# Optimization experiments

Measured on AMD Instinct MI355X. Metric: run time of the kernel, lower is better.

Reference implementation:

```python
import jax, jax.numpy as jnp
import numpy as np

NH, K = 16, 4  # num_heads, num_points


def _ln(x, g, b):
    m = x.mean(-1, keepdims=True)
    v = jnp.var(x, axis=-1, keepdims=True)
    return (x - m) / jnp.sqrt(v + 1e-5) * g + b


def setup_inputs() -> dict:
    key = jax.random.key(0)
    ks = jax.random.split(key, 12)
    B, S, D = 16, 1024, 1024
    HD = D // NH
    def lin(k, fi, fo, scale=1.0):
        return jax.random.normal(k, (fi, fo), jnp.float32) * (scale / np.sqrt(fi))
    z = lambda n: jnp.zeros((n,), jnp.float32)
    return {
        "source": jax.random.normal(ks[0], (B, S, D), jnp.float32),
        "target": jax.random.normal(ks[1], (B, S, D), jnp.float32),
        "Wq": lin(ks[2], D, D), "bq": z(D),
        "Wo1": lin(ks[3], HD, 64), "bo1": z(64),
        "Wo2": lin(ks[4], 64, 2 * K, 0.1), "bo2": z(2 * K),
        "Wa": lin(ks[5], HD, K), "ba": z(K),
        "Wv": lin(ks[6], D, D), "bv": z(D),
        "Wout": lin(ks[7], D, D), "bout": z(D),
        "gq": jnp.ones((D,), jnp.float32), "bq_ln": z(D),
        "gkv": jnp.ones((D,), jnp.float32), "bkv_ln": z(D),
        "gffn": jnp.ones((D,), jnp.float32), "bffn_ln": z(D),
        "W1": lin(ks[8], D, 4 * D), "b1": z(4 * D),
        "W2": lin(ks[9], 4 * D, D), "b2": z(D),
    }


def _forward(source, target, Wq, bq, Wo1, bo1, Wo2, bo2, Wa, ba, Wv, bv,
             Wout, bout, gq, bq_ln, gkv, bkv_ln, gffn, bffn_ln, W1, b1, W2, b2):
    B, S, D = source.shape
    HD = D // NH
    Hs = int(round(S ** 0.5)); Ws = Hs  # S = H*W square grid

    q_norm = _ln(source, gq, bq_ln)
    v_norm = _ln(target, gkv, bkv_ln)
    q = (q_norm @ Wq + bq).reshape(B, S, NH, HD)
    # value map per head: (B, NH, H, W, HD)
    v = (v_norm @ Wv + bv).reshape(B, Hs, Ws, NH, HD).transpose(0, 3, 1, 2, 4)
    v_flat = v.reshape(B, NH, Hs * Ws, HD)

    # learned offsets: tanh(MLP(q)) * 0.5, in normalized [-1,1] coords
    h = jax.nn.relu(q @ Wo1 + bo1)
    off = jnp.tanh((h @ Wo2 + bo2).reshape(B, S, NH, K, 2)) * 0.5

    # reference grid: ref_grid[i*W+j] = (ref_x[j], ref_y[i])
    rx = jnp.linspace(-1.0, 1.0, Ws)
    ry = jnp.linspace(-1.0, 1.0, Hs)
    gx, gy = jnp.meshgrid(rx, ry)  # 'xy' indexing
    ref = jnp.stack([gx, gy], -1).reshape(S, 2)
    pts = ref[None, :, None, None, :] + off  # (B, S, NH, K, 2), last dim = (x, y)

    # grid_sample, bilinear, align_corners=True, padding_mode='zeros'
    x = (pts[..., 0] + 1.0) * 0.5 * (Ws - 1)
    y = (pts[..., 1] + 1.0) * 0.5 * (Hs - 1)
    x = jnp.moveaxis(x, 1, 2)  # (B, NH, S, K)
    y = jnp.moveaxis(y, 1, 2)
    x0 = jnp.floor(x); y0 = jnp.floor(y)
    wx1 = x - x0; wy1 = y - y0
    x0i = x0.astype(jnp.int32); y0i = y0.astype(jnp.int32)

    def gather(xi, yi, w):
        m = (xi >= 0) & (xi <= Ws - 1) & (yi >= 0) & (yi <= Hs - 1)
        idx = jnp.clip(yi, 0, Hs - 1) * Ws + jnp.clip(xi, 0, Ws - 1)
        g = jnp.take_along_axis(v_flat, idx.reshape(B, NH, S * K, 1), axis=2)
        return g.reshape(B, NH, S, K, HD) * (w * m)[..., None]

    sampled = (gather(x0i, y0i, (1.0 - wx1) * (1.0 - wy1))
               + gather(x0i + 1, y0i, wx1 * (1.0 - wy1))
               + gather(x0i, y0i + 1, (1.0 - wx1) * wy1)
               + gather(x0i + 1, y0i + 1, wx1 * wy1))  # (B, NH, S, K, HD)

    attn = jax.nn.softmax(q @ Wa + ba, axis=-1)  # (B, S, NH, K)
    head_out = jnp.einsum('bsnk,bnskd->bsnd', attn, sampled).reshape(B, S, D)

    src = source + (head_out @ Wout + bout)
    f = jax.nn.gelu(_ln(src, gffn, bffn_ln) @ W1 + b1, approximate=False)
    return src + (f @ W2 + b2)


def reference(source, target, Wq, bq, Wo1, bo1, Wo2, bo2, Wa, ba, Wv, bv,
              Wout, bout, gq, bq_ln, gkv, bkv_ln, gffn, bffn_ln, W1, b1, W2, b2):
    return _forward(source, target, Wq, bq, Wo1, bo1, Wo2, bo2, Wa, ba, Wv, bv,
                    Wout, bout, gq, bq_ln, gkv, bkv_ln, gffn, bffn_ln, W1, b1, W2, b2)
```

## Files before the change

kernel.cpp:

```cpp
#include <hip/hip_runtime.h>

typedef __attribute__((ext_vector_type(8))) short short8;
typedef __attribute__((ext_vector_type(4))) float f32x4;

#define DEV __device__ __forceinline__

DEV float bf2f(unsigned short u) { return __uint_as_float(((unsigned)u) << 16); }
DEV unsigned short f2bf(float f) {
  unsigned u = __float_as_uint(f);
  u += 0x7FFF + ((u >> 16) & 1);
  return (unsigned short)(u >> 16);
}

#define GLOAD_LDS16(gptr, lptr)                                                              \
  __builtin_amdgcn_global_load_lds((const __attribute__((address_space(1))) void*)(gptr),   \
                                   (__attribute__((address_space(3))) void*)(lptr), 16, 0, 0)

__global__ __launch_bounds__(256) void wt_transpose_bf16(const float* __restrict__ W,
                                                         unsigned short* __restrict__ Wt,
                                                         int K, int N) {
  __shared__ float t[32][33];
  int k0 = blockIdx.x * 32, n0 = blockIdx.y * 32;
  int tx = threadIdx.x, ty = threadIdx.y;
#pragma unroll
  for (int i = 0; i < 4; ++i)
    t[ty + 8 * i][tx] = W[(long)(k0 + ty + 8 * i) * N + n0 + tx];
  __syncthreads();
#pragma unroll
  for (int i = 0; i < 4; ++i)
    Wt[(long)(n0 + ty + 8 * i) * K + k0 + tx] = f2bf(t[tx][ty + 8 * i]);
}

__global__ __launch_bounds__(256) void ln_to_bf16(const float* __restrict__ x,
                                                  const float* __restrict__ g,
                                                  const float* __restrict__ b,
                                                  unsigned short* __restrict__ y) {
  const long row = blockIdx.x;
  const int tid = threadIdx.x;
  float4 v = *(const float4*)(x + row * 1024 + tid * 4);
  float s = v.x + v.y + v.z + v.w;
  float s2 = v.x * v.x + v.y * v.y + v.z * v.z + v.w * v.w;
#pragma unroll
  for (int o = 32; o > 0; o >>= 1) { s += __shfl_down(s, o); s2 += __shfl_down(s2, o); }
  __shared__ float red[8];
  __shared__ float mv[2];
  int wv = tid >> 6, ln = tid & 63;
  if (ln == 0) { red[wv] = s; red[4 + wv] = s2; }
  __syncthreads();
  if (tid == 0) {
    float a = red[0] + red[1] + red[2] + red[3];
    float q = red[4] + red[5] + red[6] + red[7];
    float mean = a * (1.f / 1024.f);
    mv[0] = mean;
    mv[1] = rsqrtf(q * (1.f / 1024.f) - mean * mean + 1e-5f);
  }
  __syncthreads();
  float mean = mv[0], rstd = mv[1];
  float4 gg = *(const float4*)(g + tid * 4);
  float4 bb = *(const float4*)(b + tid * 4);
  ushort4 o;
  o.x = f2bf((v.x - mean) * rstd * gg.x + bb.x);
  o.y = f2bf((v.y - mean) * rstd * gg.y + bb.y);
  o.z = f2bf((v.z - mean) * rstd * gg.z + bb.z);
  o.w = f2bf((v.w - mean) * rstd * gg.w + bb.w);
  *(ushort4*)(y + row * 1024 + tid * 4) = o;
}

template <int EPI>
__global__ __launch_bounds__(512, 4) void gemm_bf16(const unsigned short* __restrict__ A,
                                                    const unsigned short* __restrict__ Bt,
                                                    const float* __restrict__ bias,
                                                    const float* __restrict__ res,
                                                    void* __restrict__ out,
                                                    int N, int K, int ldb) {
  __shared__ __align__(16) char smem[65536];
  const int tid = threadIdx.x;
  const int wave = tid >> 6, lane = tid & 63;
  const int wm = wave >> 2, wn = wave & 3;
  const long col0 = (long)blockIdx.x * 128;
  const long row0 = (long)blockIdx.y * 128;

  f32x4 acc[4][2];
#pragma unroll
  for (int i = 0; i < 4; ++i)
#pragma unroll
    for (int n = 0; n < 2; ++n) acc[i][n] = f32x4{0.f, 0.f, 0.f, 0.f};

  const int rin = lane >> 4, ch = lane & 15;

  for (int kt = 0; kt < K; kt += 128) {
#pragma unroll
    for (int i = 0; i < 4; ++i) {
      const int c = wave * 4 + i;
      const int r = c * 4 + rin;
      const int kg = ch ^ (r & 15);
      GLOAD_LDS16(A + (row0 + r) * (long)K + kt + kg * 8, smem + c * 1024);
      GLOAD_LDS16(Bt + (col0 + r) * (long)ldb + kt + kg * 8, smem + 32768 + c * 1024);
    }
    asm volatile("s_waitcnt vmcnt(0)" ::: "memory");
    __syncthreads();
#pragma unroll
    for (int ks = 0; ks < 4; ++ks) {
      short8 af[4], bfr[2];
#pragma unroll
      for (int i = 0; i < 4; ++i) {
        const int rowa = wm * 64 + i * 16 + (lane & 15);
        const int pc = (ks * 4 + (lane >> 4)) ^ (rowa & 15);
        af[i] = *(const short8*)(smem + rowa * 256 + pc * 16);
      }
#pragma unroll
      for (int n = 0; n < 2; ++n) {
        const int rowb = wn * 32 + n * 16 + (lane & 15);
        const int pc = (ks * 4 + (lane >> 4)) ^ (rowb & 15);
        bfr[n] = *(const short8*)(smem + 32768 + rowb * 256 + pc * 16);
      }
#pragma unroll
      for (int i = 0; i < 4; ++i)
#pragma unroll
        for (int n = 0; n < 2; ++n)
          acc[i][n] = __builtin_amdgcn_mfma_f32_16x16x32_bf16(af[i], bfr[n], acc[i][n], 0, 0, 0);
    }
    __syncthreads();
  }

  const int lr = lane >> 4, lc = lane & 15;
#pragma unroll
  for (int i = 0; i < 4; ++i) {
#pragma unroll
    for (int n = 0; n < 2; ++n) {
      const long gcol = col0 + wn * 32 + n * 16 + lc;
      const float bvv = (EPI == 5) ? 0.f : bias[gcol];
#pragma unroll
      for (int r = 0; r < 4; ++r) {
        const long grow = row0 + wm * 64 + i * 16 + lr * 4 + r;
        float val = acc[i][n][r] + bvv;
        if (EPI == 0) {
          ((float*)out)[grow * N + gcol] = val;
        } else if (EPI == 1) {
          const int b_ = (int)(grow >> 10), hw = (int)(grow & 1023);
          const int nh = (int)(gcol >> 6), hd = (int)(gcol & 63);
          ((unsigned short*)out)[((long)(b_ * 16 + nh) << 16) + hw * 64 + hd] = f2bf(val);
        } else if (EPI == 2) {
          ((float*)out)[grow * N + gcol] = val + res[grow * N + gcol];
        } else if (EPI == 3) {
          float gl = 0.5f * val * (1.f + erff(val * 0.70710678118654752f));
          ((unsigned short*)out)[grow * N + gcol] = f2bf(gl);
        } else {
          ((float*)out)[grow * N + gcol] = val + res[grow * N + gcol];
        }
      }
    }
  }
}

__global__ __launch_bounds__(256) void offset_attn_mlp(
    const float* __restrict__ qf,
    const float* __restrict__ Wo1, const float* __restrict__ bo1,
    const float* __restrict__ Wo2, const float* __restrict__ bo2,
    const float* __restrict__ Wa, const float* __restrict__ ba,
    float* __restrict__ coords) {
  const int r = blockIdx.x * 256 + threadIdx.x;
  const int s = (r >> 4) & 1023;

  float qr[64];
  const float* qp = qf + (long)r * 64;
#pragma unroll
  for (int i = 0; i < 16; ++i) *(float4*)(qr + 4 * i) = *(const float4*)(qp + 4 * i);

  float off[8];
#pragma unroll
  for (int o = 0; o < 8; ++o) off[o] = bo2[o];

#pragma unroll 1
  for (int jj = 0; jj < 8; ++jj) {
    float hacc[8];
#pragma unroll
    for (int o = 0; o < 8; ++o) hacc[o] = bo1[jj * 8 + o];
#pragma unroll
    for (int i = 0; i < 64; ++i) {
      const float qv = qr[i];
#pragma unroll
      for (int o = 0; o < 8; ++o) hacc[o] = fmaf(qv, Wo1[i * 64 + jj * 8 + o], hacc[o]);
    }
#pragma unroll
    for (int jo = 0; jo < 8; ++jo) {
      const float hj = fmaxf(hacc[jo], 0.f);
      const int j = jj * 8 + jo;
#pragma unroll
      for (int o = 0; o < 8; ++o) off[o] = fmaf(hj, Wo2[j * 8 + o], off[o]);
    }
  }

  float lg[4];
#pragma unroll
  for (int k = 0; k < 4; ++k) lg[k] = ba[k];
#pragma unroll
  for (int i = 0; i < 64; ++i) {
    const float qv = qr[i];
#pragma unroll
    for (int k = 0; k < 4; ++k) lg[k] = fmaf(qv, Wa[i * 4 + k], lg[k]);
  }
  const float mx = fmaxf(fmaxf(lg[0], lg[1]), fmaxf(lg[2], lg[3]));
  const float e0 = expf(lg[0] - mx), e1 = expf(lg[1] - mx), e2 = expf(lg[2] - mx),
              e3 = expf(lg[3] - mx);
  const float inv = 1.f / (e0 + e1 + e2 + e3);

  const float sx = (float)(s & 31), sy = (float)(s >> 5);
  float4 xv, yv, av;
  xv.x = sx + tanhf(off[0]) * 7.75f; yv.x = sy + tanhf(off[1]) * 7.75f;
  xv.y = sx + tanhf(off[2]) * 7.75f; yv.y = sy + tanhf(off[3]) * 7.75f;
  xv.z = sx + tanhf(off[4]) * 7.75f; yv.z = sy + tanhf(off[5]) * 7.75f;
  xv.w = sx + tanhf(off[6]) * 7.75f; yv.w = sy + tanhf(off[7]) * 7.75f;
  av.x = e0 * inv; av.y = e1 * inv; av.z = e2 * inv; av.w = e3 * inv;
  float* cp = coords + (long)r * 16;
  *(float4*)(cp + 0) = xv;
  *(float4*)(cp + 4) = yv;
  *(float4*)(cp + 8) = av;
}

__global__ __launch_bounds__(256) void deform_gather(
    const unsigned short* __restrict__ v_flat, const float* __restrict__ coords,
    unsigned short* __restrict__ head_out) {
  const int tid = threadIdx.x, wave = tid >> 6, lane = tid & 63;
  const int m = blockIdx.x * 4 + wave;
  const int b = m >> 14, nh = (m >> 10) & 15, s = m & 1023;
  const long r = (long)(b * 1024 + s) * 16 + nh;

  float cf = 0.f;
  if (lane < 12) cf = coords[r * 16 + lane];
  const unsigned short* vb = v_flat + ((long)(b * 16 + nh) << 16);

  float o = 0.f;
#pragma unroll
  for (int k = 0; k < 4; ++k) {
    const float xp = __shfl(cf, k), yp = __shfl(cf, 4 + k), ak = __shfl(cf, 8 + k);
    const float x0f = floorf(xp), y0f = floorf(yp);
    const int x0 = (int)x0f, y0 = (int)y0f;
    const float wx1 = xp - x0f, wy1 = yp - y0f;
    const float wx0 = 1.f - wx1, wy0 = 1.f - wy1;
    float smp = 0.f;
#pragma unroll
    for (int cn = 0; cn < 4; ++cn) {
      const int xi = x0 + (cn & 1), yi = y0 + (cn >> 1);
      const float w = (cn & 1 ? wx1 : wx0) * (cn >> 1 ? wy1 : wy0);
      const bool msk = (xi >= 0) & (xi <= 31) & (yi >= 0) & (yi <= 31);
      const int xc = min(max(xi, 0), 31), yc = min(max(yi, 0), 31);
      const float vv = bf2f(vb[(yc * 32 + xc) * 64 + lane]);
      smp = fmaf(vv, msk ? w : 0.f, smp);
    }
    o = fmaf(ak, smp, o);
  }
  head_out[r * 64 + lane] = f2bf(o);
}

extern "C" void kernel_launch(void* const* d_in, const int* in_sizes, int n_in,
                              void* d_out, int out_size, void* d_ws, size_t ws_size,
                              hipStream_t stream) {
  const float* source = (const float*)d_in[0];
  const float* target = (const float*)d_in[1];
  const float* Wq = (const float*)d_in[2];
  const float* bq = (const float*)d_in[3];
  const float* Wo1 = (const float*)d_in[4];
  const float* bo1 = (const float*)d_in[5];
  const float* Wo2 = (const float*)d_in[6];
  const float* bo2 = (const float*)d_in[7];
  const float* Wa = (const float*)d_in[8];
  const float* ba = (const float*)d_in[9];
  const float* Wv = (const float*)d_in[10];
  const float* bv = (const float*)d_in[11];
  const float* Wout = (const float*)d_in[12];
  const float* bout = (const float*)d_in[13];
  const float* gq = (const float*)d_in[14];
  const float* bq_ln = (const float*)d_in[15];
  const float* gkv = (const float*)d_in[16];
  const float* bkv_ln = (const float*)d_in[17];
  const float* gffn = (const float*)d_in[18];
  const float* bffn_ln = (const float*)d_in[19];
  const float* W1 = (const float*)d_in[20];
  const float* b1 = (const float*)d_in[21];
  const float* W2 = (const float*)d_in[22];
  const float* b2 = (const float*)d_in[23];

  char* ws = (char*)d_ws;
  const size_t MB = 1u << 20;
  if (ws_size < 150 * MB) return;

  unsigned short* q_norm = (unsigned short*)(ws + 0);
  unsigned short* v_flat = (unsigned short*)(ws + 0);
  unsigned short* v_norm = (unsigned short*)(ws + 32 * MB);
  float* coords = (float*)(ws + 32 * MB);
  unsigned short* ffn_in = (unsigned short*)(ws + 32 * MB);
  float* qf = (float*)(ws + 64 * MB);
  unsigned short* head_out = (unsigned short*)(ws + 64 * MB);
  unsigned short* f_buf = (unsigned short*)(ws + 64 * MB);
  unsigned short* Wq_t = (unsigned short*)(ws + 128 * MB);
  unsigned short* Wv_t = (unsigned short*)(ws + 130 * MB);
  unsigned short* Wout_t = (unsigned short*)(ws + 132 * MB);
  unsigned short* W1_t = (unsigned short*)(ws + 134 * MB);
  unsigned short* W2_t = (unsigned short*)(ws + 142 * MB);
  float* src = (float*)d_out;

  dim3 tb(32, 8);
  wt_transpose_bf16<<<dim3(32, 32), tb, 0, stream>>>(Wq, Wq_t, 1024, 1024);
  wt_transpose_bf16<<<dim3(32, 32), tb, 0, stream>>>(Wv, Wv_t, 1024, 1024);
  wt_transpose_bf16<<<dim3(32, 32), tb, 0, stream>>>(Wout, Wout_t, 1024, 1024);
  wt_transpose_bf16<<<dim3(32, 128), tb, 0, stream>>>(W1, W1_t, 1024, 4096);
  wt_transpose_bf16<<<dim3(128, 32), tb, 0, stream>>>(W2, W2_t, 4096, 1024);

  ln_to_bf16<<<16384, 256, 0, stream>>>(source, gq, bq_ln, q_norm);
  ln_to_bf16<<<16384, 256, 0, stream>>>(target, gkv, bkv_ln, v_norm);

  gemm_bf16<0><<<dim3(8, 128), 512, 0, stream>>>(q_norm, Wq_t, bq, nullptr, qf, 1024, 1024, 1024);
  gemm_bf16<1><<<dim3(8, 128), 512, 0, stream>>>(v_norm, Wv_t, bv, nullptr, v_flat, 1024, 1024, 1024);

  offset_attn_mlp<<<1024, 256, 0, stream>>>(qf, Wo1, bo1, Wo2, bo2, Wa, ba, coords);
  deform_gather<<<65536, 256, 0, stream>>>(v_flat, coords, head_out);

  gemm_bf16<2><<<dim3(8, 128), 512, 0, stream>>>(head_out, Wout_t, bout, source, src, 1024, 1024, 1024);

  ln_to_bf16<<<16384, 256, 0, stream>>>(src, gffn, bffn_ln, ffn_in);

  gemm_bf16<3><<<dim3(16, 128), 512, 0, stream>>>(ffn_in, W1_t, b1, nullptr, f_buf, 2048, 1024, 1024);
  gemm_bf16<2><<<dim3(8, 128), 512, 0, stream>>>(f_buf, W2_t, b2, src, src, 1024, 2048, 4096);
  gemm_bf16<3><<<dim3(16, 128), 512, 0, stream>>>(ffn_in, W1_t + (long)2048 * 1024, b1 + 2048,
                                                  nullptr, f_buf, 2048, 1024, 1024);
  gemm_bf16<5><<<dim3(8, 128), 512, 0, stream>>>(f_buf, W2_t + 2048, nullptr, src, src, 1024, 2048, 4096);
}
```

Baseline: 786.3 us.

## Switch GEMM to 32x32x16 MFMA with 256x128 tiles and BK=64

```diff
diff --git a/kernel.cpp b/kernel.cpp
--- a/kernel.cpp
+++ b/kernel.cpp
@@ -1,7 +1,7 @@
 #include <hip/hip_runtime.h>
 
 typedef __attribute__((ext_vector_type(8))) short short8;
-typedef __attribute__((ext_vector_type(4))) float f32x4;
+typedef __attribute__((ext_vector_type(16))) float f32x16;
 
 #define DEV __device__ __forceinline__
 
@@ -73,67 +73,74 @@
                                                     const float* __restrict__ res,
                                                     void* __restrict__ out,
                                                     int N, int K, int ldb) {
-  __shared__ __align__(16) char smem[65536];
+  __shared__ __align__(16) char smem[49152];
   const int tid = threadIdx.x;
   const int wave = tid >> 6, lane = tid & 63;
-  const int wm = wave >> 2, wn = wave & 3;
+  const int wm = wave >> 1, wn = wave & 1;
   const long col0 = (long)blockIdx.x * 128;
-  const long row0 = (long)blockIdx.y * 128;
-
-  f32x4 acc[4][2];
-#pragma unroll
-  for (int i = 0; i < 4; ++i)
-#pragma unroll
-    for (int n = 0; n < 2; ++n) acc[i][n] = f32x4{0.f, 0.f, 0.f, 0.f};
-
-  const int rin = lane >> 4, ch = lane & 15;
-
-  for (int kt = 0; kt < K; kt += 128) {
+  const long row0 = (long)blockIdx.y * 256;
+
+  f32x16 acc[2][2];
+#pragma unroll
+  for (int i = 0; i < 2; ++i)
+#pragma unroll
+    for (int n = 0; n < 2; ++n)
+#pragma unroll
+      for (int r = 0; r < 16; ++r) acc[i][n][r] = 0.f;
+
+  const int rin = lane >> 3, ch = lane & 7;
+  const int kg = ch ^ rin;
+
+  for (int kt = 0; kt < K; kt += 64) {
 #pragma unroll
     for (int i = 0; i < 4; ++i) {
       const int c = wave * 4 + i;
-      const int r = c * 4 + rin;
-      const int kg = ch ^ (r & 15);
+      const int r = c * 8 + rin;
       GLOAD_LDS16(A + (row0 + r) * (long)K + kt + kg * 8, smem + c * 1024);
+    }
+#pragma unroll
+    for (int i = 0; i < 2; ++i) {
+      const int c = wave * 2 + i;
+      const int r = c * 8 + rin;
       GLOAD_LDS16(Bt + (col0 + r) * (long)ldb + kt + kg * 8, smem + 32768 + c * 1024);
     }
     asm volatile("s_waitcnt vmcnt(0)" ::: "memory");
     __syncthreads();
 #pragma unroll
     for (int ks = 0; ks < 4; ++ks) {
-      short8 af[4], bfr[2];
-#pragma unroll
-      for (int i = 0; i < 4; ++i) {
-        const int rowa = wm * 64 + i * 16 + (lane & 15);
-        const int pc = (ks * 4 + (lane >> 4)) ^ (rowa & 15);
-        af[i] = *(const short8*)(smem + rowa * 256 + pc * 16);
+      short8 af[2], bfr[2];
+      const int kc = ks * 2 + (lane >> 5);
+#pragma unroll
+      for (int mi = 0; mi < 2; ++mi) {
+        const int rowa = wm * 64 + mi * 32 + (lane & 31);
+        af[mi] = *(const short8*)(smem + rowa * 128 + (kc ^ (rowa & 7)) * 16);
       }
 #pragma unroll
-      for (int n = 0; n < 2; ++n) {
-        const int rowb = wn * 32 + n * 16 + (lane & 15);
-        const int pc = (ks * 4 + (lane >> 4)) ^ (rowb & 15);
-        bfr[n] = *(const short8*)(smem + 32768 + rowb * 256 + pc * 16);
+      for (int ni = 0; ni < 2; ++ni) {
+        const int rowb = wn * 64 + ni * 32 + (lane & 31);
+        bfr[ni] = *(const short8*)(smem + 32768 + rowb * 128 + (kc ^ (rowb & 7)) * 16);
       }
 #pragma unroll
-      for (int i = 0; i < 4; ++i)
-#pragma unroll
-        for (int n = 0; n < 2; ++n)
-          acc[i][n] = __builtin_amdgcn_mfma_f32_16x16x32_bf16(af[i], bfr[n], acc[i][n], 0, 0, 0);
+      for (int mi = 0; mi < 2; ++mi)
+#pragma unroll
+        for (int ni = 0; ni < 2; ++ni)
+          acc[mi][ni] =
+              __builtin_amdgcn_mfma_f32_32x32x16_bf16(af[mi], bfr[ni], acc[mi][ni], 0, 0, 0);
     }
     __syncthreads();
   }
 
-  const int lr = lane >> 4, lc = lane & 15;
-#pragma unroll
-  for (int i = 0; i < 4; ++i) {
-#pragma unroll
-    for (int n = 0; n < 2; ++n) {
-      const long gcol = col0 + wn * 32 + n * 16 + lc;
+  const int lc = lane & 31, lh = lane >> 5;
+#pragma unroll
+  for (int mi = 0; mi < 2; ++mi) {
+#pragma unroll
+    for (int ni = 0; ni < 2; ++ni) {
+      const long gcol = col0 + wn * 64 + ni * 32 + lc;
       const float bvv = (EPI == 5) ? 0.f : bias[gcol];
 #pragma unroll
-      for (int r = 0; r < 4; ++r) {
-        const long grow = row0 + wm * 64 + i * 16 + lr * 4 + r;
-        float val = acc[i][n][r] + bvv;
+      for (int reg = 0; reg < 16; ++reg) {
+        const long grow = row0 + wm * 64 + mi * 32 + (reg & 3) + 8 * (reg >> 2) + 4 * lh;
+        float val = acc[mi][ni][reg] + bvv;
         if (EPI == 0) {
           ((float*)out)[grow * N + gcol] = val;
         } else if (EPI == 1) {
@@ -310,19 +317,19 @@
   ln_to_bf16<<<16384, 256, 0, stream>>>(source, gq, bq_ln, q_norm);
   ln_to_bf16<<<16384, 256, 0, stream>>>(target, gkv, bkv_ln, v_norm);
 
-  gemm_bf16<0><<<dim3(8, 128), 512, 0, stream>>>(q_norm, Wq_t, bq, nullptr, qf, 1024, 1024, 1024);
-  gemm_bf16<1><<<dim3(8, 128), 512, 0, stream>>>(v_norm, Wv_t, bv, nullptr, v_flat, 1024, 1024, 1024);
+  gemm_bf16<0><<<dim3(8, 64), 512, 0, stream>>>(q_norm, Wq_t, bq, nullptr, qf, 1024, 1024, 1024);
+  gemm_bf16<1><<<dim3(8, 64), 512, 0, stream>>>(v_norm, Wv_t, bv, nullptr, v_flat, 1024, 1024, 1024);
 
   offset_attn_mlp<<<1024, 256, 0, stream>>>(qf, Wo1, bo1, Wo2, bo2, Wa, ba, coords);
   deform_gather<<<65536, 256, 0, stream>>>(v_flat, coords, head_out);
 
-  gemm_bf16<2><<<dim3(8, 128), 512, 0, stream>>>(head_out, Wout_t, bout, source, src, 1024, 1024, 1024);
+  gemm_bf16<2><<<dim3(8, 64), 512, 0, stream>>>(head_out, Wout_t, bout, source, src, 1024, 1024, 1024);
 
   ln_to_bf16<<<16384, 256, 0, stream>>>(src, gffn, bffn_ln, ffn_in);
 
-  gemm_bf16<3><<<dim3(16, 128), 512, 0, stream>>>(ffn_in, W1_t, b1, nullptr, f_buf, 2048, 1024, 1024);
-  gemm_bf16<2><<<dim3(8, 128), 512, 0, stream>>>(f_buf, W2_t, b2, src, src, 1024, 2048, 4096);
-  gemm_bf16<3><<<dim3(16, 128), 512, 0, stream>>>(ffn_in, W1_t + (long)2048 * 1024, b1 + 2048,
-                                                  nullptr, f_buf, 2048, 1024, 1024);
-  gemm_bf16<5><<<dim3(8, 128), 512, 0, stream>>>(f_buf, W2_t + 2048, nullptr, src, src, 1024, 2048, 4096);
-}
+  gemm_bf16<3><<<dim3(16, 64), 512, 0, stream>>>(ffn_in, W1_t, b1, nullptr, f_buf, 2048, 1024, 1024);
+  gemm_bf16<2><<<dim3(8, 64), 512, 0, stream>>>(f_buf, W2_t, b2, src, src, 1024, 2048, 4096);
+  gemm_bf16<3><<<dim3(16, 64), 512, 0, stream>>>(ffn_in, W1_t + (long)2048 * 1024, b1 + 2048,
+                                                 nullptr, f_buf, 2048, 1024, 1024);
+  gemm_bf16<5><<<dim3(8, 64), 512, 0, stream>>>(f_buf, W2_t + 2048, nullptr, src, src, 1024, 2048, 4096);
+}
```

New measurement: 766.6 us. -2.5%, faster.

## Add 256x128 GEMM using 32x32x16 MFMA and unsplit FFN when workspace allows

Applied to the files above, without the earlier changes.

```diff
diff --git a/kernel.cpp b/kernel.cpp
--- a/kernel.cpp
+++ b/kernel.cpp
@@ -2,6 +2,7 @@
 
 typedef __attribute__((ext_vector_type(8))) short short8;
 typedef __attribute__((ext_vector_type(4))) float f32x4;
+typedef __attribute__((ext_vector_type(16))) float f32x16;
 
 #define DEV __device__ __forceinline__
 
@@ -64,6 +65,24 @@
   o.z = f2bf((v.z - mean) * rstd * gg.z + bb.z);
   o.w = f2bf((v.w - mean) * rstd * gg.w + bb.w);
   *(ushort4*)(y + row * 1024 + tid * 4) = o;
+}
+
+template <int EPI>
+DEV void epi_store(void* out, const float* res, long grow, long gcol, int N, float val) {
+  if (EPI == 0) {
+    ((float*)out)[grow * N + gcol] = val;
+  } else if (EPI == 1) {
+    const int b_ = (int)(grow >> 10), hw = (int)(grow & 1023);
+    const int nh = (int)(gcol >> 6), hd = (int)(gcol & 63);
+    ((unsigned short*)out)[((long)(b_ * 16 + nh) << 16) + hw * 64 + hd] = f2bf(val);
+  } else if (EPI == 2) {
+    ((float*)out)[grow * N + gcol] = val + res[grow * N + gcol];
+  } else if (EPI == 3) {
+    float gl = 0.5f * val * (1.f + erff(val * 0.70710678118654752f));
+    ((unsigned short*)out)[grow * N + gcol] = f2bf(gl);
+  } else {
+    ((float*)out)[grow * N + gcol] = val + res[grow * N + gcol];
+  }
 }
 
 template <int EPI>
@@ -125,7 +144,7 @@
 
   const int lr = lane >> 4, lc = lane & 15;
 #pragma unroll
-  for (int i = 0; i < 4; ++i) {
+  for (int i = 0; i < 4; ++i)
 #pragma unroll
     for (int n = 0; n < 2; ++n) {
       const long gcol = col0 + wn * 32 + n * 16 + lc;
@@ -133,24 +152,89 @@
 #pragma unroll
       for (int r = 0; r < 4; ++r) {
         const long grow = row0 + wm * 64 + i * 16 + lr * 4 + r;
-        float val = acc[i][n][r] + bvv;
-        if (EPI == 0) {
-          ((float*)out)[grow * N + gcol] = val;
-        } else if (EPI == 1) {
-          const int b_ = (int)(grow >> 10), hw = (int)(grow & 1023);
-          const int nh = (int)(gcol >> 6), hd = (int)(gcol & 63);
-          ((unsigned short*)out)[((long)(b_ * 16 + nh) << 16) + hw * 64 + hd] = f2bf(val);
-        } else if (EPI == 2) {
-          ((float*)out)[grow * N + gcol] = val + res[grow * N + gcol];
-        } else if (EPI == 3) {
-          float gl = 0.5f * val * (1.f + erff(val * 0.70710678118654752f));
-          ((unsigned short*)out)[grow * N + gcol] = f2bf(gl);
-        } else {
-          ((float*)out)[grow * N + gcol] = val + res[grow * N + gcol];
-        }
-      }
-    }
-  }
+        epi_store<EPI>(out, res, grow, gcol, N, acc[i][n][r] + bvv);
+      }
+    }
+}
+
+template <int EPI>
+__global__ __launch_bounds__(512, 4) void gemm32(const unsigned short* __restrict__ A,
+                                                 const unsigned short* __restrict__ Bt,
+                                                 const float* __restrict__ bias,
+                                                 const float* __restrict__ res,
+                                                 void* __restrict__ out,
+                                                 int N, int K, int ldb) {
+  __shared__ __align__(16) char smem[49152];
+  const int tid = threadIdx.x;
+  const int wave = tid >> 6, lane = tid & 63;
+  const int wm = wave >> 1, wn = wave & 1;
+  const long col0 = (long)blockIdx.x * 128;
+  const long row0 = (long)blockIdx.y * 256;
+
+  f32x16 acc[2][2];
+#pragma unroll
+  for (int i = 0; i < 2; ++i)
+#pragma unroll
+    for (int n = 0; n < 2; ++n)
+#pragma unroll
+      for (int r = 0; r < 16; ++r) acc[i][n][r] = 0.f;
+
+  const int rin = lane >> 3, ch = lane & 7;
+
+  for (int kt = 0; kt < K; kt += 64) {
+#pragma unroll
+    for (int i = 0; i < 4; ++i) {
+      const int c = wave * 4 + i;
+      const int r = c * 8 + rin;
+      const int kg = ch ^ ((r >> 1) & 7);
+      GLOAD_LDS16(A + (row0 + r) * (long)K + kt + kg * 8, smem + c * 1024);
+    }
+#pragma unroll
+    for (int i = 0; i < 2; ++i) {
+      const int c = wave * 2 + i;
+      const int r = c * 8 + rin;
+      const int kg = ch ^ ((r >> 1) & 7);
+      GLOAD_LDS16(Bt + (col0 + r) * (long)ldb + kt + kg * 8, smem + 32768 + c * 1024);
+    }
+    asm volatile("s_waitcnt vmcnt(0)" ::: "memory");
+    __syncthreads();
+#pragma unroll
+    for (int ks = 0; ks < 4; ++ks) {
+      short8 af[2], bfr[2];
+      const int kc = ks * 2 + (lane >> 5);
+#pragma unroll
+      for (int mi = 0; mi < 2; ++mi) {
+        const int rowa = wm * 64 + mi * 32 + (lane & 31);
+        af[mi] = *(const short8*)(smem + rowa * 128 + (kc ^ ((rowa >> 1) & 7)) * 16);
+      }
+#pragma unroll
+      for (int ni = 0; ni < 2; ++ni) {
+        const int rowb = wn * 64 + ni * 32 + (lane & 31);
+        bfr[ni] = *(const short8*)(smem + 32768 + rowb * 128 + (kc ^ ((rowb >> 1) & 7)) * 16);
+      }
+#pragma unroll
+      for (int mi = 0; mi < 2; ++mi)
+#pragma unroll
+        for (int ni = 0; ni < 2; ++ni)
+          acc[mi][ni] =
+              __builtin_amdgcn_mfma_f32_32x32x16_bf16(af[mi], bfr[ni], acc[mi][ni], 0, 0, 0);
+    }
+    __syncthreads();
+  }
+
+  const int lc = lane & 31, lh = lane >> 5;
+#pragma unroll
+  for (int mi = 0; mi < 2; ++mi)
+#pragma unroll
+    for (int ni = 0; ni < 2; ++ni) {
+      const long gcol = col0 + wn * 64 + ni * 32 + lc;
+      const float bvv = (EPI == 5) ? 0.f : bias[gcol];
+#pragma unroll
+      for (int reg = 0; reg < 16; ++reg) {
+        const long grow = row0 + wm * 64 + mi * 32 + (reg & 3) + 8 * (reg >> 2) + 4 * lh;
+        epi_store<EPI>(out, res, grow, gcol, N, acc[mi][ni][reg] + bvv);
+      }
+    }
 }
 
 __global__ __launch_bounds__(256) void offset_attn_mlp(
@@ -284,20 +368,22 @@
   char* ws = (char*)d_ws;
   const size_t MB = 1u << 20;
   if (ws_size < 150 * MB) return;
+  const bool big = (ws_size >= 182 * MB);
 
   unsigned short* q_norm = (unsigned short*)(ws + 0);
   unsigned short* v_flat = (unsigned short*)(ws + 0);
   unsigned short* v_norm = (unsigned short*)(ws + 32 * MB);
   float* coords = (float*)(ws + 32 * MB);
-  unsigned short* ffn_in = (unsigned short*)(ws + 32 * MB);
   float* qf = (float*)(ws + 64 * MB);
   unsigned short* head_out = (unsigned short*)(ws + 64 * MB);
-  unsigned short* f_buf = (unsigned short*)(ws + 64 * MB);
-  unsigned short* Wq_t = (unsigned short*)(ws + 128 * MB);
-  unsigned short* Wv_t = (unsigned short*)(ws + 130 * MB);
-  unsigned short* Wout_t = (unsigned short*)(ws + 132 * MB);
-  unsigned short* W1_t = (unsigned short*)(ws + 134 * MB);
-  unsigned short* W2_t = (unsigned short*)(ws + 142 * MB);
+  unsigned short* ffn_in = (unsigned short*)(big ? ws + 128 * MB : ws + 32 * MB);
+  unsigned short* f_buf = (unsigned short*)(big ? ws + 0 : ws + 64 * MB);
+  char* wbase = big ? ws + 160 * MB : ws + 128 * MB;
+  unsigned short* Wq_t = (unsigned short*)(wbase + 0);
+  unsigned short* Wv_t = (unsigned short*)(wbase + 2 * MB);
+  unsigned short* Wout_t = (unsigned short*)(wbase + 4 * MB);
+  unsigned short* W1_t = (unsigned short*)(wbase + 6 * MB);
+  unsigned short* W2_t = (unsigned short*)(wbase + 14 * MB);
   float* src = (float*)d_out;
 
   dim3 tb(32, 8);
@@ -310,19 +396,24 @@
   ln_to_bf16<<<16384, 256, 0, stream>>>(source, gq, bq_ln, q_norm);
   ln_to_bf16<<<16384, 256, 0, stream>>>(target, gkv, bkv_ln, v_norm);
 
-  gemm_bf16<0><<<dim3(8, 128), 512, 0, stream>>>(q_norm, Wq_t, bq, nullptr, qf, 1024, 1024, 1024);
-  gemm_bf16<1><<<dim3(8, 128), 512, 0, stream>>>(v_norm, Wv_t, bv, nullptr, v_flat, 1024, 1024, 1024);
+  gemm32<0><<<dim3(8, 64), 512, 0, stream>>>(q_norm, Wq_t, bq, nullptr, qf, 1024, 1024, 1024);
+  gemm32<1><<<dim3(8, 64), 512, 0, stream>>>(v_norm, Wv_t, bv, nullptr, v_flat, 1024, 1024, 1024);
 
   offset_attn_mlp<<<1024, 256, 0, stream>>>(qf, Wo1, bo1, Wo2, bo2, Wa, ba, coords);
   deform_gather<<<65536, 256, 0, stream>>>(v_flat, coords, head_out);
 
-  gemm_bf16<2><<<dim3(8, 128), 512, 0, stream>>>(head_out, Wout_t, bout, source, src, 1024, 1024, 1024);
+  gemm32<2><<<dim3(8, 64), 512, 0, stream>>>(head_out, Wout_t, bout, source, src, 1024, 1024, 1024);
 
   ln_to_bf16<<<16384, 256, 0, stream>>>(src, gffn, bffn_ln, ffn_in);
 
-  gemm_bf16<3><<<dim3(16, 128), 512, 0, stream>>>(ffn_in, W1_t, b1, nullptr, f_buf, 2048, 1024, 1024);
-  gemm_bf16<2><<<dim3(8, 128), 512, 0, stream>>>(f_buf, W2_t, b2, src, src, 1024, 2048, 4096);
-  gemm_bf16<3><<<dim3(16, 128), 512, 0, stream>>>(ffn_in, W1_t + (long)2048 * 1024, b1 + 2048,
-                                                  nullptr, f_buf, 2048, 1024, 1024);
-  gemm_bf16<5><<<dim3(8, 128), 512, 0, stream>>>(f_buf, W2_t + 2048, nullptr, src, src, 1024, 2048, 4096);
-}
+  if (big) {
+    gemm32<3><<<dim3(32, 64), 512, 0, stream>>>(ffn_in, W1_t, b1, nullptr, f_buf, 4096, 1024, 1024);
+    gemm_bf16<2><<<dim3(8, 128), 512, 0, stream>>>(f_buf, W2_t, b2, src, src, 1024, 4096, 4096);
+  } else {
+    gemm32<3><<<dim3(16, 64), 512, 0, stream>>>(ffn_in, W1_t, b1, nullptr, f_buf, 2048, 1024, 1024);
+    gemm_bf16<2><<<dim3(8, 128), 512, 0, stream>>>(f_buf, W2_t, b2, src, src, 1024, 2048, 4096);
+    gemm32<3><<<dim3(16, 64), 512, 0, stream>>>(ffn_in, W1_t + (long)2048 * 1024, b1 + 2048,
+                                                nullptr, f_buf, 2048, 1024, 1024);
+    gemm_bf16<5><<<dim3(8, 128), 512, 0, stream>>>(f_buf, W2_t + 2048, nullptr, src, src, 1024, 2048, 4096);
+  }
+}
```

Measured after the change: 736.8 us. -6.3%, faster.
